# Performance work log

Measured on AMD Instinct MI355X. Metric: run time of the kernel, lower is better.

The kernel has to match this reference:

```python
import jax, jax.numpy as jnp
import numpy as np

EPS_POS = 1e-6  # eps passed explicitly for positive cosine_similarity
EPS_NEG = 1e-8  # torch default eps for negative cosine_similarity


def setup_inputs() -> dict:
    key = jax.random.key(0)
    dvectors = jax.random.normal(key, (1024, 32, 256), dtype=jnp.float32)
    w = jnp.array([10.0], dtype=jnp.float32)
    b = jnp.array([-5.0], dtype=jnp.float32)
    return {"dvectors": dvectors, "w": w, "b": b}


def reference(dvectors, w, b):
    S, U, D = dvectors.shape

    # ---- positive: leave-one-out centroid within each speaker ----
    # pos_centroid[s,u] = mean of speaker s's utterances excluding u
    pos_cent = (dvectors.sum(axis=1, keepdims=True) - dvectors) / (U - 1)  # [S,U,D]
    dn_pos = dvectors / jnp.maximum(
        jnp.linalg.norm(dvectors, axis=-1, keepdims=True), EPS_POS)
    cn_pos = pos_cent / jnp.maximum(
        jnp.linalg.norm(pos_cent, axis=-1, keepdims=True), EPS_POS)
    pos_cos = jnp.sum(dn_pos * cn_pos, axis=-1)  # [S,U]

    # ---- negative: full (non-LOO) centroids of every speaker ----
    cent = dvectors.mean(axis=1)  # [S,D]
    dn = dvectors / jnp.maximum(
        jnp.linalg.norm(dvectors, axis=-1, keepdims=True), EPS_NEG)
    cn = cent / jnp.maximum(jnp.linalg.norm(cent, axis=-1, keepdims=True), EPS_NEG)
    all_cos = jnp.einsum('sud,td->sut', dn, cn)  # [S,U,S] cos(dvec[s,u], cent[t])

    # own-speaker entries all_cos[s,u,s] are EXCLUDED from neg_sim
    own = jnp.take_along_axis(
        all_cos, jnp.arange(S, dtype=jnp.int32)[:, None, None], axis=2
    ).squeeze(2)  # [S,U]

    pos_mean = jnp.mean(pos_cos)
    neg_mean = (jnp.sum(all_cos) - jnp.sum(own)) / (S * U * (S - 1))

    # scaled sims: w * cos + b  (torch.clamp(self.w, 1e-6) in forward is a no-op)
    w0 = w[0]
    b0 = b[0]
    pos_scaled = w0 * pos_cos + b0  # [S,U]
    neg_scaled = w0 * all_cos + b0  # [S,U,S]

    # logsumexp over the S-1 other speakers (mask own speaker to -inf)
    own_mask = jnp.eye(S, dtype=bool)[:, None, :]  # [S,1,S]
    neg_masked = jnp.where(own_mask, -jnp.inf, neg_scaled)
    lse = jax.nn.logsumexp(neg_masked, axis=2)  # [S,U]

    loss = jnp.mean(-pos_scaled + lse)
    return (loss, pos_mean, neg_mean)
```

## Files before the change

kernel.cpp:

```cpp
#include <hip/hip_runtime.h>
#include <math.h>

#define NS 1024
#define NU 32
#define ND 256
#define BROWS 128
#define NBLK ((NS * NU) / BROWS)

static constexpr float EPS_POS = 1e-6f;
static constexpr float EPS_NEG = 1e-8f;

typedef __attribute__((ext_vector_type(8))) short bf16x8;
typedef __attribute__((ext_vector_type(4))) float f32x4;

#if __has_builtin(__builtin_amdgcn_exp2f)
#define EXP2F(x) __builtin_amdgcn_exp2f(x)
#else
#define EXP2F(x) exp2f(x)
#endif

static __device__ __forceinline__ unsigned short f2bf(float f) {
    union { float f; unsigned u; } v; v.f = f;
    unsigned r = v.u + 0x7fffu + ((v.u >> 16) & 1u);
    return (unsigned short)(r >> 16);
}

__global__ __launch_bounds__(256) void ge2e_k1(
    const float* __restrict__ dv, unsigned short* __restrict__ cnb,
    float* __restrict__ invn, float* __restrict__ blk_pos)
{
    const int s = blockIdx.x;
    const int tid = threadIdx.x;
    const int wave = tid >> 6;
    const int lane = tid & 63;

    __shared__ float v[NU][ND];
    __shared__ float cs[ND];
    __shared__ float red[16];

    const float* base = dv + (size_t)s * (NU * ND);
    for (int idx = tid; idx < NU * ND; idx += 256) {
        v[idx >> 8][idx & 255] = base[idx];
    }
    __syncthreads();

    {
        float a = 0.f;
        #pragma unroll
        for (int u = 0; u < NU; ++u) a += v[u][tid];
        cs[tid] = a;
    }
    __syncthreads();

    float c = cs[tid] * (1.0f / NU);
    float p = c * c;
    #pragma unroll
    for (int off = 32; off > 0; off >>= 1) p += __shfl_xor(p, off, 64);
    if (lane == 0) red[wave] = p;
    __syncthreads();
    if (tid == 0) red[8] = red[0] + red[1] + red[2] + red[3];
    __syncthreads();
    {
        float rn = 1.0f / fmaxf(sqrtf(red[8]), EPS_NEG);
        cnb[(size_t)s * ND + tid] = f2bf(c * rn);
    }

    const float inv31 = 1.0f / (NU - 1);
    float pos_part = 0.f;
    const float4 cc = *(const float4*)&cs[lane * 4];
    for (int uu = 0; uu < 8; ++uu) {
        const int u = wave * 8 + uu;
        const float4 vv = *(const float4*)&v[u][lane * 4];
        float pv = 0.f, pp = 0.f, px = 0.f;
        float pc;
        pc = (cc.x - vv.x) * inv31; pv += vv.x * vv.x; pp += pc * pc; px += vv.x * pc;
        pc = (cc.y - vv.y) * inv31; pv += vv.y * vv.y; pp += pc * pc; px += vv.y * pc;
        pc = (cc.z - vv.z) * inv31; pv += vv.z * vv.z; pp += pc * pc; px += vv.z * pc;
        pc = (cc.w - vv.w) * inv31; pv += vv.w * vv.w; pp += pc * pc; px += vv.w * pc;
        #pragma unroll
        for (int off = 32; off > 0; off >>= 1) {
            pv += __shfl_xor(pv, off, 64);
            pp += __shfl_xor(pp, off, 64);
            px += __shfl_xor(px, off, 64);
        }
        if (lane == 0) {
            float nv = sqrtf(pv), npc = sqrtf(pp);
            pos_part += px / (fmaxf(nv, EPS_POS) * fmaxf(npc, EPS_POS));
            invn[s * NU + u] = 1.0f / fmaxf(nv, EPS_NEG);
        }
    }
    if (lane == 0) red[4 + wave] = pos_part;
    __syncthreads();
    if (tid == 0) blk_pos[s] = red[4] + red[5] + red[6] + red[7];
}

__global__ __launch_bounds__(512, 2) void ge2e_k2(
    const float* __restrict__ dv, const unsigned short* __restrict__ cnb,
    const float* __restrict__ invn, const float* __restrict__ wp,
    const float* __restrict__ bp, float* __restrict__ blk_neg,
    float* __restrict__ blk_lse)
{
    const int b  = blockIdx.x;
    const int r0 = b * BROWS;
    const int tid = threadIdx.x;
    const int w  = tid >> 6;
    const int l  = tid & 63;
    const int lr = l & 15;
    const int lg = l >> 4;
    const int mg = w >> 2;
    const int ng = w & 3;

    __shared__ unsigned short Al[BROWS][264];
    __shared__ unsigned short Bst[2][4][16][256];
    __shared__ float sinv[BROWS];
    __shared__ float pse[4][BROWS];
    __shared__ float psm[4][BROWS];
    __shared__ float redn[2], redl[2];

    const float w0 = wp[0];
    const float b0 = bp[0];
    const float c2 = w0 * 1.4426950408889634f;

    if (tid < BROWS) sinv[tid] = invn[r0 + tid];

    size_t srcb[4];
    unsigned ldso[4];
    #pragma unroll
    for (int i = 0; i < 4; ++i) {
        const int gi = w * 256 + i * 64 + l;
        const int ngs = gi >> 9, g = gi & 511, rrs = g >> 5, gcs = g & 31;
        srcb[i] = (size_t)((ngs * 256 + rrs) * 32 + (gcs ^ (rrs & 7))) * 16;
        ldso[i] = (unsigned)(w * 256 + i * 64) * 16;
    }
    const char* cnbc = (const char*)cnb;

    #pragma unroll
    for (int i = 0; i < 4; ++i) {
        __builtin_amdgcn_global_load_lds(
            (const __attribute__((address_space(1))) void*)(cnbc + srcb[i]),
            (__attribute__((address_space(3))) void*)((char*)&Bst[0][0][0][0] + ldso[i]),
            16, 0, 0);
    }
    __syncthreads();

    #pragma unroll
    for (int r = 0; r < 8; ++r) {
        const int i = tid + r * 512;
        const int row = i >> 5, g = i & 31;
        const float* src = dv + (size_t)(r0 + row) * ND + g * 8;
        const float4 x = *(const float4*)src;
        const float4 y = *(const float4*)(src + 4);
        const float sc = sinv[row];
        uint4 pk;
        pk.x = (unsigned)f2bf(x.x * sc) | ((unsigned)f2bf(x.y * sc) << 16);
        pk.y = (unsigned)f2bf(x.z * sc) | ((unsigned)f2bf(x.w * sc) << 16);
        pk.z = (unsigned)f2bf(y.x * sc) | ((unsigned)f2bf(y.y * sc) << 16);
        pk.w = (unsigned)f2bf(y.z * sc) | ((unsigned)f2bf(y.w * sc) << 16);
        *(uint4*)&Al[row][g * 8] = pk;
    }
    __syncthreads();

    bf16x8 afr[4][8];
    #pragma unroll
    for (int mt = 0; mt < 4; ++mt)
        #pragma unroll
        for (int kt = 0; kt < 8; ++kt)
            afr[mt][kt] = *(const bf16x8*)&Al[mg * 64 + mt * 16 + lr][kt * 32 + lg * 8];

    float se[4][4], sm[4][4];
    #pragma unroll
    for (int mt = 0; mt < 4; ++mt)
        #pragma unroll
        for (int r = 0; r < 4; ++r) { se[mt][r] = 0.f; sm[mt][r] = 0.f; }

    const int rsw = lr & 7;
    int town[4];
    #pragma unroll
    for (int mt = 0; mt < 4; ++mt) town[mt] = (r0 + mg * 64 + mt * 16) >> 5;

    #pragma unroll 2
    for (int j = 0; j < 16; ++j) {
        if (j < 15) {
            char* bdst = (char*)&Bst[(j + 1) & 1][0][0][0];
            const size_t soff = (size_t)(j + 1) * 8192;
            #pragma unroll
            for (int i = 0; i < 4; ++i) {
                __builtin_amdgcn_global_load_lds(
                    (const __attribute__((address_space(1))) void*)(cnbc + srcb[i] + soff),
                    (__attribute__((address_space(3))) void*)(bdst + ldso[i]),
                    16, 0, 0);
            }
        }

        const unsigned short (*bc)[16][256] = Bst[j & 1];
        f32x4 acc[4];
        #pragma unroll
        for (int mt = 0; mt < 4; ++mt) acc[mt] = (f32x4){0.f, 0.f, 0.f, 0.f};

        #pragma unroll
        for (int kt = 0; kt < 8; ++kt) {
            const bf16x8 bfr = *(const bf16x8*)&bc[ng][lr][(((kt * 4 + lg) ^ rsw)) * 8];
            #pragma unroll
            for (int mt = 0; mt < 4; ++mt)
                acc[mt] = __builtin_amdgcn_mfma_f32_16x16x32_bf16(afr[mt][kt], bfr, acc[mt], 0, 0, 0);
        }

        #pragma unroll
        for (int mt = 0; mt < 4; ++mt)
            #pragma unroll
            for (int r = 0; r < 4; ++r) {
                const float cv = acc[mt][r];
                se[mt][r] += EXP2F(fmaf(c2, cv, -c2));
                sm[mt][r] += cv;
            }

        #pragma unroll
        for (int mt = 0; mt < 4; ++mt) {
            if (ng == (town[mt] >> 8) && j == ((town[mt] >> 4) & 15)) {
                if (lr == (town[mt] & 15)) {
                    #pragma unroll
                    for (int r = 0; r < 4; ++r) {
                        const float cv = acc[mt][r];
                        se[mt][r] -= EXP2F(fmaf(c2, cv, -c2));
                        sm[mt][r] -= cv;
                    }
                }
            }
        }

        __syncthreads();
    }

    #pragma unroll
    for (int mask = 1; mask <= 8; mask <<= 1)
        #pragma unroll
        for (int mt = 0; mt < 4; ++mt)
            #pragma unroll
            for (int r = 0; r < 4; ++r) {
                se[mt][r] += __shfl_xor(se[mt][r], mask, 64);
                sm[mt][r] += __shfl_xor(sm[mt][r], mask, 64);
            }

    if (lr == 0) {
        #pragma unroll
        for (int mt = 0; mt < 4; ++mt)
            #pragma unroll
            for (int r = 0; r < 4; ++r) {
                const int row = mg * 64 + mt * 16 + lg * 4 + r;
                pse[ng][row] = se[mt][r];
                psm[ng][row] = sm[mt][r];
            }
    }
    __syncthreads();

    if (tid < BROWS) {
        float st = 0.f, smt = 0.f;
        #pragma unroll
        for (int q = 0; q < 4; ++q) { st += pse[q][tid]; smt += psm[q][tid]; }
        float lse = w0 + b0 + __logf(st);
        #pragma unroll
        for (int mask = 1; mask <= 32; mask <<= 1) {
            lse += __shfl_xor(lse, mask, 64);
            smt += __shfl_xor(smt, mask, 64);
        }
        if ((tid & 63) == 0) { redn[tid >> 6] = smt; redl[tid >> 6] = lse; }
    }
    __syncthreads();
    if (tid == 0) {
        blk_neg[b] = redn[0] + redn[1];
        blk_lse[b] = redl[0] + redl[1];
    }
}

__global__ __launch_bounds__(256) void ge2e_k3(
    const float* __restrict__ blk_pos, const float* __restrict__ blk_neg,
    const float* __restrict__ blk_lse, const float* __restrict__ wp,
    const float* __restrict__ bp, float* __restrict__ out)
{
    const int tid = threadIdx.x;
    __shared__ float red[12];
    float p = 0.f, n = 0.f, l = 0.f;
    for (int i = tid; i < NS; i += 256) p += blk_pos[i];
    if (tid < NBLK) { n = blk_neg[tid]; l = blk_lse[tid]; }
    #pragma unroll
    for (int off = 32; off > 0; off >>= 1) {
        p += __shfl_xor(p, off, 64);
        n += __shfl_xor(n, off, 64);
        l += __shfl_xor(l, off, 64);
    }
    const int wave = tid >> 6, lane = tid & 63;
    if (lane == 0) { red[wave] = p; red[4 + wave] = n; red[8 + wave] = l; }
    __syncthreads();
    if (tid == 0) {
        const float ps = red[0] + red[1] + red[2] + red[3];
        const float ns = red[4] + red[5] + red[6] + red[7];
        const float ls = red[8] + red[9] + red[10] + red[11];
        const float pos_mean = ps * (1.0f / (NS * NU));
        const float neg_mean = ns / ((float)NS * (float)NU * (float)(NS - 1));
        const float lse_mean = ls * (1.0f / (NS * NU));
        const float loss = -(wp[0] * pos_mean + bp[0]) + lse_mean;
        out[0] = loss;
        out[1] = pos_mean;
        out[2] = neg_mean;
    }
}

extern "C" void kernel_launch(void* const* d_in, const int* in_sizes, int n_in,
                              void* d_out, int out_size, void* d_ws, size_t ws_size,
                              hipStream_t stream)
{
    const float* dv = (const float*)d_in[0];
    const float* w  = (const float*)d_in[1];
    const float* b  = (const float*)d_in[2];
    float* out = (float*)d_out;

    unsigned short* cnb = (unsigned short*)d_ws;
    float* invn    = (float*)(cnb + (size_t)NS * ND);
    float* blk_pos = invn + NS * NU;
    float* blk_neg = blk_pos + NS;
    float* blk_lse = blk_neg + NBLK;

    hipLaunchKernelGGL(ge2e_k1, dim3(NS), dim3(256), 0, stream,
                       dv, cnb, invn, blk_pos);
    hipLaunchKernelGGL(ge2e_k2, dim3(NBLK), dim3(512), 0, stream,
                       dv, cnb, invn, w, b, blk_neg, blk_lse);
    hipLaunchKernelGGL(ge2e_k3, dim3(1), dim3(256), 0, stream,
                       blk_pos, blk_neg, blk_lse, w, b, out);
}
```

Measured before the change: 50.25 us.

## Split centroid dimension across two blocks with larger row tiles

The similarity GEMM is retiled so each block covers 256 rows and half of the 1024 centroids (two N-halves per row tile). A fragments now load straight from global memory into registers, with no LDS staging. Per-row exp sums are written out per N-half, and the final kernel combines the halves and takes the log over all 32K rows. This halves the centroid streaming per block and removes the A-side LDS round trip. In exchange, each row's dvector is read and converted twice, there is an extra partial-sum array in global memory, and the single-block final kernel now does 32K logs.

```diff
diff --git a/kernel.cpp b/kernel.cpp
--- a/kernel.cpp
+++ b/kernel.cpp
@@ -4,8 +4,10 @@
 #define NS 1024
 #define NU 32
 #define ND 256
-#define BROWS 128
-#define NBLK ((NS * NU) / BROWS)
+#define NROWS (NS * NU)
+#define BM 256
+#define BN 512
+#define NBLK ((NROWS / BM) * (NS / BN))
 
 static constexpr float EPS_POS = 1e-6f;
 static constexpr float EPS_NEG = 1e-8f;
@@ -97,94 +99,88 @@
 __global__ __launch_bounds__(512, 2) void ge2e_k2(
     const float* __restrict__ dv, const unsigned short* __restrict__ cnb,
     const float* __restrict__ invn, const float* __restrict__ wp,
-    const float* __restrict__ bp, float* __restrict__ blk_neg,
-    float* __restrict__ blk_lse)
+    const float* __restrict__ bp, float* __restrict__ rowse,
+    float* __restrict__ blk_neg)
 {
-    const int b  = blockIdx.x;
-    const int r0 = b * BROWS;
+    const int blk = blockIdx.x;
+    const int bm = blk >> 1;
+    const int bn = blk & 1;
+    const int r0 = bm * BM;
     const int tid = threadIdx.x;
     const int w  = tid >> 6;
     const int l  = tid & 63;
     const int lr = l & 15;
     const int lg = l >> 4;
-    const int mg = w >> 2;
-    const int ng = w & 3;
-
-    __shared__ unsigned short Al[BROWS][264];
-    __shared__ unsigned short Bst[2][4][16][256];
-    __shared__ float sinv[BROWS];
-    __shared__ float pse[4][BROWS];
-    __shared__ float psm[4][BROWS];
-    __shared__ float redn[2], redl[2];
+    const int mg = w & 3;
+    const int ng = w >> 2;
+    const int rsw = lr & 7;
+
+    __shared__ unsigned short Bst[2][32][256];
+    __shared__ float pse[2][BM];
+    __shared__ float psm[2][BM];
+    __shared__ float redn[8];
 
     const float w0 = wp[0];
-    const float b0 = bp[0];
     const float c2 = w0 * 1.4426950408889634f;
 
-    if (tid < BROWS) sinv[tid] = invn[r0 + tid];
-
-    size_t srcb[4];
-    unsigned ldso[4];
-    #pragma unroll
-    for (int i = 0; i < 4; ++i) {
-        const int gi = w * 256 + i * 64 + l;
-        const int ngs = gi >> 9, g = gi & 511, rrs = g >> 5, gcs = g & 31;
-        srcb[i] = (size_t)((ngs * 256 + rrs) * 32 + (gcs ^ (rrs & 7))) * 16;
-        ldso[i] = (unsigned)(w * 256 + i * 64) * 16;
+    size_t srcb[2];
+    unsigned ldso[2];
+    #pragma unroll
+    for (int i = 0; i < 2; ++i) {
+        const int gi = w * 128 + i * 64 + l;
+        const int rr = gi >> 5;
+        const int gc = gi & 31;
+        const int t0 = bn * 512 + (rr >> 4) * 256 + (rr & 15);
+        srcb[i] = (size_t)t0 * 512 + (size_t)(gc ^ (rr & 7)) * 16;
+        ldso[i] = (unsigned)(w * 128 + i * 64) * 16;
     }
     const char* cnbc = (const char*)cnb;
 
     #pragma unroll
-    for (int i = 0; i < 4; ++i) {
+    for (int i = 0; i < 2; ++i) {
         __builtin_amdgcn_global_load_lds(
             (const __attribute__((address_space(1))) void*)(cnbc + srcb[i]),
-            (__attribute__((address_space(3))) void*)((char*)&Bst[0][0][0][0] + ldso[i]),
+            (__attribute__((address_space(3))) void*)((char*)&Bst[0][0][0] + ldso[i]),
             16, 0, 0);
     }
-    __syncthreads();
-
-    #pragma unroll
-    for (int r = 0; r < 8; ++r) {
-        const int i = tid + r * 512;
-        const int row = i >> 5, g = i & 31;
-        const float* src = dv + (size_t)(r0 + row) * ND + g * 8;
-        const float4 x = *(const float4*)src;
-        const float4 y = *(const float4*)(src + 4);
-        const float sc = sinv[row];
-        uint4 pk;
-        pk.x = (unsigned)f2bf(x.x * sc) | ((unsigned)f2bf(x.y * sc) << 16);
-        pk.y = (unsigned)f2bf(x.z * sc) | ((unsigned)f2bf(x.w * sc) << 16);
-        pk.z = (unsigned)f2bf(y.x * sc) | ((unsigned)f2bf(y.y * sc) << 16);
-        pk.w = (unsigned)f2bf(y.z * sc) | ((unsigned)f2bf(y.w * sc) << 16);
-        *(uint4*)&Al[row][g * 8] = pk;
-    }
-    __syncthreads();
 
     bf16x8 afr[4][8];
     #pragma unroll
+    for (int mt = 0; mt < 4; ++mt) {
+        const int grow = r0 + mg * 64 + mt * 16 + lr;
+        const float sc = invn[grow];
+        const float* rbase = dv + (size_t)grow * ND;
+        #pragma unroll
+        for (int kt = 0; kt < 8; ++kt) {
+            const float4 x = *(const float4*)(rbase + kt * 32 + lg * 8);
+            const float4 y = *(const float4*)(rbase + kt * 32 + lg * 8 + 4);
+            uint4 pk;
+            pk.x = (unsigned)f2bf(x.x * sc) | ((unsigned)f2bf(x.y * sc) << 16);
+            pk.y = (unsigned)f2bf(x.z * sc) | ((unsigned)f2bf(x.w * sc) << 16);
+            pk.z = (unsigned)f2bf(y.x * sc) | ((unsigned)f2bf(y.y * sc) << 16);
+            pk.w = (unsigned)f2bf(y.z * sc) | ((unsigned)f2bf(y.w * sc) << 16);
+            afr[mt][kt] = *(bf16x8*)&pk;
+        }
+    }
+
+    float se[4][4], sm[4][4];
+    #pragma unroll
     for (int mt = 0; mt < 4; ++mt)
         #pragma unroll
-        for (int kt = 0; kt < 8; ++kt)
-            afr[mt][kt] = *(const bf16x8*)&Al[mg * 64 + mt * 16 + lr][kt * 32 + lg * 8];
-
-    float se[4][4], sm[4][4];
-    #pragma unroll
-    for (int mt = 0; mt < 4; ++mt)
-        #pragma unroll
         for (int r = 0; r < 4; ++r) { se[mt][r] = 0.f; sm[mt][r] = 0.f; }
 
-    const int rsw = lr & 7;
     int town[4];
     #pragma unroll
     for (int mt = 0; mt < 4; ++mt) town[mt] = (r0 + mg * 64 + mt * 16) >> 5;
 
-    #pragma unroll 2
     for (int j = 0; j < 16; ++j) {
+        __syncthreads();
+
         if (j < 15) {
-            char* bdst = (char*)&Bst[(j + 1) & 1][0][0][0];
+            char* bdst = (char*)&Bst[(j + 1) & 1][0][0];
             const size_t soff = (size_t)(j + 1) * 8192;
             #pragma unroll
-            for (int i = 0; i < 4; ++i) {
+            for (int i = 0; i < 2; ++i) {
                 __builtin_amdgcn_global_load_lds(
                     (const __attribute__((address_space(1))) void*)(cnbc + srcb[i] + soff),
                     (__attribute__((address_space(3))) void*)(bdst + ldso[i]),
@@ -192,14 +188,14 @@
             }
         }
 
-        const unsigned short (*bc)[16][256] = Bst[j & 1];
+        const unsigned short (*bc)[256] = Bst[j & 1];
         f32x4 acc[4];
         #pragma unroll
         for (int mt = 0; mt < 4; ++mt) acc[mt] = (f32x4){0.f, 0.f, 0.f, 0.f};
 
         #pragma unroll
         for (int kt = 0; kt < 8; ++kt) {
-            const bf16x8 bfr = *(const bf16x8*)&bc[ng][lr][(((kt * 4 + lg) ^ rsw)) * 8];
+            const bf16x8 bfr = *(const bf16x8*)&bc[ng * 16 + lr][(((kt * 4 + lg)) ^ rsw) * 8];
             #pragma unroll
             for (int mt = 0; mt < 4; ++mt)
                 acc[mt] = __builtin_amdgcn_mfma_f32_16x16x32_bf16(afr[mt][kt], bfr, acc[mt], 0, 0, 0);
@@ -216,8 +212,9 @@
 
         #pragma unroll
         for (int mt = 0; mt < 4; ++mt) {
-            if (ng == (town[mt] >> 8) && j == ((town[mt] >> 4) & 15)) {
-                if (lr == (town[mt] & 15)) {
+            const int tn = town[mt];
+            if ((tn >> 9) == bn && ((tn >> 8) & 1) == ng && ((tn >> 4) & 15) == j) {
+                if (lr == (tn & 15)) {
                     #pragma unroll
                     for (int r = 0; r < 4; ++r) {
                         const float cv = acc[mt][r];
@@ -227,8 +224,6 @@
                 }
             }
         }
-
-        __syncthreads();
     }
 
     #pragma unroll
@@ -253,35 +248,32 @@
     }
     __syncthreads();
 
-    if (tid < BROWS) {
-        float st = 0.f, smt = 0.f;
-        #pragma unroll
-        for (int q = 0; q < 4; ++q) { st += pse[q][tid]; smt += psm[q][tid]; }
-        float lse = w0 + b0 + __logf(st);
-        #pragma unroll
-        for (int mask = 1; mask <= 32; mask <<= 1) {
-            lse += __shfl_xor(lse, mask, 64);
+    if (tid < BM) {
+        rowse[(size_t)bn * NROWS + r0 + tid] = pse[0][tid] + pse[1][tid];
+        float smt = psm[0][tid] + psm[1][tid];
+        #pragma unroll
+        for (int mask = 1; mask <= 32; mask <<= 1)
             smt += __shfl_xor(smt, mask, 64);
-        }
-        if ((tid & 63) == 0) { redn[tid >> 6] = smt; redl[tid >> 6] = lse; }
-    }
-    __syncthreads();
-    if (tid == 0) {
-        blk_neg[b] = redn[0] + redn[1];
-        blk_lse[b] = redl[0] + redl[1];
-    }
-}
-
-__global__ __launch_bounds__(256) void ge2e_k3(
+        if ((tid & 63) == 0) redn[tid >> 6] = smt;
+    }
+    __syncthreads();
+    if (tid == 0) blk_neg[blk] = redn[0] + redn[1] + redn[2] + redn[3];
+}
+
+__global__ __launch_bounds__(1024) void ge2e_k3(
     const float* __restrict__ blk_pos, const float* __restrict__ blk_neg,
-    const float* __restrict__ blk_lse, const float* __restrict__ wp,
+    const float* __restrict__ rowse, const float* __restrict__ wp,
     const float* __restrict__ bp, float* __restrict__ out)
 {
     const int tid = threadIdx.x;
-    __shared__ float red[12];
+    __shared__ float red[48];
+
     float p = 0.f, n = 0.f, l = 0.f;
-    for (int i = tid; i < NS; i += 256) p += blk_pos[i];
-    if (tid < NBLK) { n = blk_neg[tid]; l = blk_lse[tid]; }
+    if (tid < NS) p = blk_pos[tid];
+    if (tid < NBLK) n = blk_neg[tid];
+    for (int r = tid; r < NROWS; r += 1024)
+        l += __logf(rowse[r] + rowse[NROWS + r]);
+
     #pragma unroll
     for (int off = 32; off > 0; off >>= 1) {
         p += __shfl_xor(p, off, 64);
@@ -289,16 +281,20 @@
         l += __shfl_xor(l, off, 64);
     }
     const int wave = tid >> 6, lane = tid & 63;
-    if (lane == 0) { red[wave] = p; red[4 + wave] = n; red[8 + wave] = l; }
+    if (lane == 0) { red[wave] = p; red[16 + wave] = n; red[32 + wave] = l; }
     __syncthreads();
     if (tid == 0) {
-        const float ps = red[0] + red[1] + red[2] + red[3];
-        const float ns = red[4] + red[5] + red[6] + red[7];
-        const float ls = red[8] + red[9] + red[10] + red[11];
-        const float pos_mean = ps * (1.0f / (NS * NU));
+        float ps = 0.f, ns = 0.f, ls = 0.f;
+        #pragma unroll
+        for (int q = 0; q < 16; ++q) {
+            ps += red[q]; ns += red[16 + q]; ls += red[32 + q];
+        }
+        const float w0 = wp[0];
+        const float b0 = bp[0];
+        const float pos_mean = ps * (1.0f / NROWS);
         const float neg_mean = ns / ((float)NS * (float)NU * (float)(NS - 1));
-        const float lse_mean = ls * (1.0f / (NS * NU));
-        const float loss = -(wp[0] * pos_mean + bp[0]) + lse_mean;
+        const float lse_mean = w0 + b0 + ls * (1.0f / NROWS);
+        const float loss = -(w0 * pos_mean + b0) + lse_mean;
         out[0] = loss;
         out[1] = pos_mean;
         out[2] = neg_mean;
@@ -316,14 +312,14 @@
 
     unsigned short* cnb = (unsigned short*)d_ws;
     float* invn    = (float*)(cnb + (size_t)NS * ND);
-    float* blk_pos = invn + NS * NU;
+    float* blk_pos = invn + NROWS;
     float* blk_neg = blk_pos + NS;
-    float* blk_lse = blk_neg + NBLK;
+    float* rowse   = blk_neg + NBLK;
 
     hipLaunchKernelGGL(ge2e_k1, dim3(NS), dim3(256), 0, stream,
                        dv, cnb, invn, blk_pos);
     hipLaunchKernelGGL(ge2e_k2, dim3(NBLK), dim3(512), 0, stream,
-                       dv, cnb, invn, w, b, blk_neg, blk_lse);
-    hipLaunchKernelGGL(ge2e_k3, dim3(1), dim3(256), 0, stream,
-                       blk_pos, blk_neg, blk_lse, w, b, out);
-}
+                       dv, cnb, invn, w, b, rowse, blk_neg);
+    hipLaunchKernelGGL(ge2e_k3, dim3(1), dim3(1024), 0, stream,
+                       blk_pos, blk_neg, rowse, w, b, out);
+}
```

Result: slower. 68.57 us (+36.5%).
